# Optimization experiments

Measured on AMD Instinct MI355X. Metric: run time of the kernel, lower is better.

Reference implementation:

```python
import jax, jax.numpy as jnp
import numpy as np

D_MODEL = 512
D_STATE = 16
D_CONV = 4
EXPAND = 2
HEADDIM = 64
D_INNER = EXPAND * D_MODEL            # 1024
NHEADS = D_INNER // HEADDIM           # 16
CONV_DIM = D_INNER + 2 * D_STATE      # 1056 (x, B, C channels)
D_IN_PROJ = 2 * D_INNER + 2 * D_STATE + NHEADS  # 2096
EPS = 1e-5
B_SZ, L_SEQ = 8, 4096


def _mamba_param_keys(prefix):
    return [prefix + n for n in
            ('in_proj', 'conv_w', 'conv_b', 'dt_bias', 'A_log', 'D', 'norm_w', 'out_proj')]


def _make_mamba_params(key, prefix):
    ks = jax.random.split(key, 4)
    s = 0.02
    return {
        prefix + 'in_proj': jax.random.normal(ks[0], (D_IN_PROJ, D_MODEL), jnp.float32) * s,
        prefix + 'conv_w': jax.random.normal(ks[1], (CONV_DIM, D_CONV), jnp.float32) * s,
        prefix + 'conv_b': jnp.zeros((CONV_DIM,), jnp.float32),
        prefix + 'dt_bias': jax.random.normal(ks[2], (NHEADS,), jnp.float32) * 0.1,
        prefix + 'A_log': jnp.log(jnp.arange(1, NHEADS + 1, dtype=jnp.float32)),
        prefix + 'D': jnp.ones((NHEADS,), jnp.float32),
        prefix + 'norm_w': jnp.ones((D_INNER,), jnp.float32),
        prefix + 'out_proj': jax.random.normal(ks[3], (D_MODEL, D_INNER), jnp.float32) * s,
    }


def setup_inputs() -> dict:
    key = jax.random.key(0)
    kx, kf, kb, kp = jax.random.split(key, 4)
    inp = {'x': jax.random.normal(kx, (B_SZ, L_SEQ, D_MODEL), jnp.float32)}
    inp.update(_make_mamba_params(kf, 'f_'))
    inp.update(_make_mamba_params(kb, 'b_'))
    kp1, kp2 = jax.random.split(kp)
    inp['proj_w'] = jax.random.normal(kp1, (D_MODEL, 2 * D_MODEL), jnp.float32) * 0.02
    inp['proj_b'] = jnp.zeros((D_MODEL,), jnp.float32)
    inp['ln_w'] = jnp.ones((D_MODEL,), jnp.float32)
    inp['ln_b'] = jnp.zeros((D_MODEL,), jnp.float32)
    return inp


def mamba2(x, in_proj, conv_w, conv_b, dt_bias, A_log, Dp, norm_w, out_proj):
    """Mamba2 block (ngroups=1): in_proj -> causal depthwise conv -> selective scan -> gated RMSNorm -> out_proj."""
    B, L, _ = x.shape
    zxbcdt = x @ in_proj.T                               # [B,L,2096]
    z = zxbcdt[..., :D_INNER]                            # gate
    xBC = zxbcdt[..., D_INNER:D_INNER + CONV_DIM]
    dt = jax.nn.softplus(zxbcdt[..., D_INNER + CONV_DIM:] + dt_bias)  # [B,L,H]
    # causal depthwise conv over (x, B, C) channels + SiLU
    xp = jnp.pad(xBC, ((0, 0), (D_CONV - 1, 0), (0, 0)))
    conv = conv_b + sum(xp[:, k:k + L, :] * conv_w[:, k] for k in range(D_CONV))
    xBC = jax.nn.silu(conv)
    xs = xBC[..., :D_INNER].reshape(B, L, NHEADS, HEADDIM)  # [B,L,H,P]
    Bm = xBC[..., D_INNER:D_INNER + D_STATE]                # [B,L,N]
    Cm = xBC[..., D_INNER + D_STATE:]                       # [B,L,N]
    A = -jnp.exp(A_log)                                     # [H]
    dA = jnp.exp(dt * A)                                    # [B,L,H]

    def step(h, inp):
        dA_t, dt_t, x_t, B_t, C_t = inp                     # [B,H],[B,H],[B,H,P],[B,N],[B,N]
        h = h * dA_t[..., None, None] + (dt_t[..., None] * x_t)[..., None] * B_t[:, None, None, :]
        y = jnp.einsum('bhpn,bn->bhp', h, C_t)
        return h, y

    h0 = jnp.zeros((B, NHEADS, HEADDIM, D_STATE), x.dtype)
    inps = (dA.transpose(1, 0, 2), dt.transpose(1, 0, 2), xs.transpose(1, 0, 2, 3),
            Bm.transpose(1, 0, 2), Cm.transpose(1, 0, 2))
    _, ys = jax.lax.scan(step, h0, inps)                    # ys: [L,B,H,P]
    y = ys.transpose(1, 0, 2, 3) + Dp[:, None] * xs         # skip connection
    y = y.reshape(B, L, D_INNER)
    # gated RMSNorm (norm_before_gate=False)
    y = y * jax.nn.silu(z)
    y = y * jax.lax.rsqrt(jnp.mean(y * y, axis=-1, keepdims=True) + EPS) * norm_w
    return y @ out_proj.T


def _layer_norm(x, w, b):
    mu = jnp.mean(x, axis=-1, keepdims=True)
    v = jnp.var(x, axis=-1, keepdims=True)
    return (x - mu) * jax.lax.rsqrt(v + EPS) * w + b


def reference(x,
              f_in_proj, f_conv_w, f_conv_b, f_dt_bias, f_A_log, f_D, f_norm_w, f_out_proj,
              b_in_proj, b_conv_w, b_conv_b, b_dt_bias, b_A_log, b_D, b_norm_w, b_out_proj,
              proj_w, proj_b, ln_w, ln_b):
    x_fwd = mamba2(x, f_in_proj, f_conv_w, f_conv_b, f_dt_bias, f_A_log, f_D, f_norm_w, f_out_proj)
    x_bwd = jnp.flip(
        mamba2(jnp.flip(x, axis=1), b_in_proj, b_conv_w, b_conv_b, b_dt_bias, b_A_log, b_D, b_norm_w, b_out_proj),
        axis=1)
    comb = jnp.concatenate([x_fwd, x_bwd], axis=-1)         # [B,L,2D]
    out = comb @ proj_w.T + proj_b                          # dropout is identity (eval / p=0)
    return _layer_norm(x + out, ln_w, ln_b)
```

## Files before the change

kernel.cpp:

```cpp
#include <hip/hip_runtime.h>
#include <hip/hip_bf16.h>
#include <math.h>

typedef __bf16 bf16x8_t __attribute__((ext_vector_type(8)));
typedef float f32x4_t __attribute__((ext_vector_type(4)));
typedef unsigned short u16x8_t __attribute__((ext_vector_type(8)));
typedef unsigned short u16x4_t __attribute__((ext_vector_type(4)));

#define DEV __device__ __forceinline__

DEV float bf2f(unsigned short u) {
    unsigned int v = ((unsigned int)u) << 16;
    return __builtin_bit_cast(float, v);
}
DEV unsigned short f2bf(float f) {
    unsigned int u = __builtin_bit_cast(unsigned int, f);
    u += 0x7fffu + ((u >> 16) & 1u);
    return (unsigned short)(u >> 16);
}

__global__ __launch_bounds__(256) void cvt_k(
    const float* __restrict__ in, unsigned short* __restrict__ out, int n8)
{
    int t = blockIdx.x * 256 + threadIdx.x;
    if (t >= n8) return;
    f32x4_t a = ((const f32x4_t*)in)[t * 2];
    f32x4_t b = ((const f32x4_t*)in)[t * 2 + 1];
    u16x8_t o;
#pragma unroll
    for (int j = 0; j < 4; j++) { o[j] = f2bf(a[j]); o[4 + j] = f2bf(b[j]); }
    ((u16x8_t*)out)[t] = o;
}

template <bool FLIP_A, bool FLIP_C, bool OUT_F32, bool ADD_BIAS, bool ACCUM>
__global__ __launch_bounds__(256, 2) void gemm_bt(
    const unsigned short* __restrict__ A,
    const unsigned short* __restrict__ W,
    void* __restrict__ Cout,
    const float* __restrict__ bias,
    int N, int K, int ldc, int col_ofs)
{
    __shared__ __attribute__((aligned(16))) unsigned char smem[16384];
    const int tid  = threadIdx.x;
    const int wave = tid >> 6;
    const int lane = tid & 63;
    const int mtile = blockIdx.y << 7;
    const int ntile = blockIdx.x << 7;

    const int c0 = tid, c1 = 256 + tid;
    const int r0 = c0 >> 2, p0 = c0 & 3, g0 = p0 ^ ((r0 >> 1) & 3);
    const int r1 = c1 >> 2, p1 = c1 & 3, g1 = p1 ^ ((r1 >> 1) & 3);

    int am0 = mtile + r0; if (FLIP_A) am0 ^= 4095;
    int am1 = mtile + r1; if (FLIP_A) am1 ^= 4095;
    const unsigned short* aP0 = A + (size_t)am0 * K + g0 * 8;
    const unsigned short* aP1 = A + (size_t)am1 * K + g1 * 8;

    int wr0 = ntile + r0; if (wr0 > N - 1) wr0 = N - 1;
    int wr1 = ntile + r1; if (wr1 > N - 1) wr1 = N - 1;
    const unsigned short* wP0 = W + (size_t)wr0 * K + g0 * 8;
    const unsigned short* wP1 = W + (size_t)wr1 * K + g1 * 8;

    unsigned char* ldsA = smem;
    unsigned char* ldsW = smem + 8192;
    unsigned char* ldsA0 = ldsA + wave * 1024;
    unsigned char* ldsA1 = ldsA + 4096 + wave * 1024;
    unsigned char* ldsW0 = ldsW + wave * 1024;
    unsigned char* ldsW1 = ldsW + 4096 + wave * 1024;

    f32x4_t acc[4][4] = {};

    const int wm = (wave & 1) << 6;
    const int wn = (wave >> 1) << 6;
    const int r    = lane & 15;
    const int quad = lane >> 4;
    const int sw   = (r >> 1) & 3;

    int aoff[4], woff[4];
#pragma unroll
    for (int i = 0; i < 4; i++) {
        int m = wm + i * 16 + r;
        aoff[i] = (m * 4 + (quad ^ sw)) * 16;
        int n = wn + i * 16 + r;
        woff[i] = (n * 4 + (quad ^ sw)) * 16;
    }

    for (int k0 = 0; k0 < K; k0 += 32) {
        __builtin_amdgcn_global_load_lds(
            (const __attribute__((address_space(1))) void*)(aP0 + k0),
            (__attribute__((address_space(3))) void*)ldsA0, 16, 0, 0);
        __builtin_amdgcn_global_load_lds(
            (const __attribute__((address_space(1))) void*)(aP1 + k0),
            (__attribute__((address_space(3))) void*)ldsA1, 16, 0, 0);
        __builtin_amdgcn_global_load_lds(
            (const __attribute__((address_space(1))) void*)(wP0 + k0),
            (__attribute__((address_space(3))) void*)ldsW0, 16, 0, 0);
        __builtin_amdgcn_global_load_lds(
            (const __attribute__((address_space(1))) void*)(wP1 + k0),
            (__attribute__((address_space(3))) void*)ldsW1, 16, 0, 0);
        __syncthreads();

        bf16x8_t af[4], wf[4];
#pragma unroll
        for (int i = 0; i < 4; i++)
            af[i] = __builtin_bit_cast(bf16x8_t, *(const u16x8_t*)(ldsA + aoff[i]));
#pragma unroll
        for (int j = 0; j < 4; j++)
            wf[j] = __builtin_bit_cast(bf16x8_t, *(const u16x8_t*)(ldsW + woff[j]));
#pragma unroll
        for (int i = 0; i < 4; i++)
#pragma unroll
            for (int j = 0; j < 4; j++)
                acc[i][j] = __builtin_amdgcn_mfma_f32_16x16x32_bf16(af[i], wf[j], acc[i][j], 0, 0, 0);
        __syncthreads();
    }

#pragma unroll
    for (int i = 0; i < 4; i++) {
#pragma unroll
        for (int j = 0; j < 4; j++) {
            int cc = ntile + wn + j * 16 + r;
            if (cc >= N) continue;
#pragma unroll
            for (int reg = 0; reg < 4; reg++) {
                int rr = mtile + wm + i * 16 + quad * 4 + reg;
                int orow = FLIP_C ? (rr ^ 4095) : rr;
                float v = acc[i][j][reg];
                if (ADD_BIAS) v += bias[cc];
                if (OUT_F32) {
                    float* p = (float*)Cout + (size_t)orow * ldc + col_ofs + cc;
                    if (ACCUM) v += *p;
                    *p = v;
                } else {
                    ((unsigned short*)Cout)[(size_t)orow * ldc + col_ofs + cc] = f2bf(v);
                }
            }
        }
    }
}

__global__ __launch_bounds__(256) void eprep2_k(
    const float* __restrict__ pw,
    const float* __restrict__ op0,
    const float* __restrict__ op1,
    unsigned short* __restrict__ E)
{
    const int dir = blockIdx.y;
    const int n0  = blockIdx.x << 2;
    const int k4  = threadIdx.x;
    const float* op  = dir ? op1 : op0;
    const float* pwr = pw + (size_t)n0 * 1024 + (dir ? 512 : 0);
    const float* opc = op + (k4 << 2);

    float acc[4][4] = {};
#pragma unroll 8
    for (int j = 0; j < 512; j++) {
        f32x4_t o = *(const f32x4_t*)(opc + ((size_t)j << 10));
        float w0 = pwr[j];
        float w1 = pwr[1024 + j];
        float w2 = pwr[2048 + j];
        float w3 = pwr[3072 + j];
#pragma unroll
        for (int q = 0; q < 4; q++) {
            acc[0][q] = fmaf(w0, o[q], acc[0][q]);
            acc[1][q] = fmaf(w1, o[q], acc[1][q]);
            acc[2][q] = fmaf(w2, o[q], acc[2][q]);
            acc[3][q] = fmaf(w3, o[q], acc[3][q]);
        }
    }

    unsigned short* Ed = E + (size_t)dir * 512 * 1024;
#pragma unroll
    for (int i = 0; i < 4; i++) {
        u16x4_t e;
#pragma unroll
        for (int q = 0; q < 4; q++) e[q] = f2bf(acc[i][q]);
        *(u16x4_t*)(Ed + (size_t)(n0 + i) * 1024 + (k4 << 2)) = e;
    }
}

__global__ __launch_bounds__(256) void conv_silu_k(
    const unsigned short* __restrict__ xin,
    const float* __restrict__ cw,
    const float* __restrict__ cb,
    unsigned short* __restrict__ outp)
{
    int t = blockIdx.x * 256 + threadIdx.x;
    int c8 = t % 132;
    int rb = t / 132;
    int c = c8 * 8;
    int row0 = rb * 8;
    int l0 = row0 & 4095;

    float w[8][4];
#pragma unroll
    for (int j = 0; j < 8; j++) {
        f32x4_t wv = *(const f32x4_t*)(cw + (c + j) * 4);
        w[j][0] = wv[0]; w[j][1] = wv[1]; w[j][2] = wv[2]; w[j][3] = wv[3];
    }
    float bia[8];
    {
        f32x4_t b0 = *(const f32x4_t*)(cb + c);
        f32x4_t b1 = *(const f32x4_t*)(cb + c + 4);
#pragma unroll
        for (int j = 0; j < 4; j++) { bia[j] = b0[j]; bia[4 + j] = b1[j]; }
    }

    u16x8_t zero;
#pragma unroll
    for (int j = 0; j < 8; j++) zero[j] = 0;

    u16x8_t win[11];
#pragma unroll
    for (int u = 0; u < 11; u++) {
        int lu = l0 - 3 + u;
        win[u] = (lu >= 0)
            ? *(const u16x8_t*)(xin + (size_t)(row0 - 3 + u) * 1072 + c)
            : zero;
    }

#pragma unroll
    for (int s = 0; s < 8; s++) {
        float acc[8];
#pragma unroll
        for (int j = 0; j < 8; j++) acc[j] = bia[j];
#pragma unroll
        for (int k = 0; k < 4; k++) {
            u16x8_t xv = win[s + k];
#pragma unroll
            for (int j = 0; j < 8; j++)
                acc[j] = fmaf(bf2f(xv[j]), w[j][k], acc[j]);
        }
        u16x8_t o;
#pragma unroll
        for (int j = 0; j < 8; j++) {
            float xx = acc[j];
            o[j] = f2bf(xx * __builtin_amdgcn_rcpf(1.f + __expf(-xx)));
        }
        *(u16x8_t*)(outp + (size_t)(row0 + s) * 1056 + c) = o;
    }
}

__global__ __launch_bounds__(256) void dt_pre_k(
    const unsigned short* __restrict__ xin,
    const float* __restrict__ dt_bias,
    const float* __restrict__ A_log,
    float* __restrict__ dtb, float* __restrict__ ldab)
{
    int t = blockIdx.x * 256 + threadIdx.x;
    int h = t & 15;
    int row = t >> 4;
    float x = bf2f(xin[(size_t)row * 1072 + 1056 + h]) + dt_bias[h];
    float dt = (x > 20.f) ? x : log1pf(__expf(x));
    float A = -__expf(A_log[h]);
    dtb[t] = dt;
    ldab[t] = dt * A;
}

DEV void stage_xt(const unsigned short* __restrict__ xrow, unsigned short* XtW, int l)
{
    u16x8_t xv[8];
#pragma unroll
    for (int m = 0; m < 8; m++) xv[m] = *(const u16x8_t*)(xrow + m * 8);
#pragma unroll
    for (int p = 0; p < 64; p++) {
        int blkc = (l >> 3) ^ (p & 7);
        XtW[p * 64 + blkc * 8 + (l & 7)] = xv[p >> 3][p & 7];
    }
}

DEV bf16x8_t xt_frag(const unsigned short* XtW, int r, int quad, int jj, int kk)
{
    int p = jj * 16 + r;
    int blkc = (kk * 4 + quad) ^ (p & 7);
    return __builtin_bit_cast(bf16x8_t, *(const u16x8_t*)(XtW + p * 64 + blkc * 8));
}

__global__ __launch_bounds__(256) void scan_chstate_k(
    const unsigned short* __restrict__ xc,
    const float* __restrict__ dtb,
    float* __restrict__ lcs,
    float* __restrict__ Hend, float* __restrict__ dec)
{
    __shared__ __attribute__((aligned(16))) unsigned char sm[37120];
    unsigned short* Btr = (unsigned short*)sm;
    float* csW = (float*)(sm + 2304);
    float* dtW = (float*)(sm + 3328);
    unsigned short* Xt0 = (unsigned short*)(sm + 4352);

    const int tid = threadIdx.x;
    const int w = tid >> 6, l = tid & 63;
    const int r = l & 15, quad = l >> 4;
    const int row0 = blockIdx.x * 64;
    const int b = blockIdx.x >> 6, chunk = blockIdx.x & 63;
    const int h = blockIdx.y * 4 + w;
    const int blk = ((b * 16 + h) << 6) | chunk;

    {
        int n = tid & 15, s0 = (tid >> 4) * 4;
#pragma unroll
        for (int js = 0; js < 4; js++) {
            int s = s0 + js;
            Btr[n * 72 + s] = xc[(size_t)(row0 + s) * 1056 + 1024 + n];
        }
    }

    float v   = lcs[(size_t)(row0 + l) * 16 + h];
    float dtv = dtb[(size_t)(row0 + l) * 16 + h];
#pragma unroll
    for (int d = 1; d < 64; d <<= 1) {
        float o = __shfl_up(v, d, 64);
        if (l >= d) v += o;
    }
    lcs[(size_t)(row0 + l) * 16 + h] = v;
    csW[w * 64 + l] = v;
    dtW[w * 64 + l] = dtv;
    if (l == 63) dec[blk] = __expf(v);
    __syncthreads();

    unsigned short* XtW = Xt0 + w * 4096;
    stage_xt(xc + (size_t)(row0 + l) * 1056 + h * 64, XtW, l);

    const float* csr = csW + w * 64;
    const float* dtr = dtW + w * 64;
    float cs63 = csr[63];

    f32x4_t z = {0.f, 0.f, 0.f, 0.f};
    f32x4_t hacc[4] = {z, z, z, z};
#pragma unroll
    for (int kk = 0; kk < 2; kk++) {
        int sb = kk * 32 + quad * 8;
        u16x8_t bv = *(const u16x8_t*)(Btr + r * 72 + sb);
        f32x4_t c0 = *(const f32x4_t*)(csr + sb);
        f32x4_t c1 = *(const f32x4_t*)(csr + sb + 4);
        f32x4_t d0 = *(const f32x4_t*)(dtr + sb);
        f32x4_t d1 = *(const f32x4_t*)(dtr + sb + 4);
        u16x8_t wv;
#pragma unroll
        for (int j = 0; j < 4; j++) {
            wv[j]     = f2bf(bf2f(bv[j])     * d0[j] * __expf(cs63 - c0[j]));
            wv[4 + j] = f2bf(bf2f(bv[4 + j]) * d1[j] * __expf(cs63 - c1[j]));
        }
        bf16x8_t wf = __builtin_bit_cast(bf16x8_t, wv);
#pragma unroll
        for (int jj = 0; jj < 4; jj++)
            hacc[jj] = __builtin_amdgcn_mfma_f32_16x16x32_bf16(wf, xt_frag(XtW, r, quad, jj, kk), hacc[jj], 0, 0, 0);
    }
    float* o = Hend + (size_t)blk * 1024;
#pragma unroll
    for (int jj = 0; jj < 4; jj++)
#pragma unroll
        for (int reg = 0; reg < 4; reg++)
            o[(jj * 16 + r) * 16 + quad * 4 + reg] = hacc[jj][reg];
}

__global__ __launch_bounds__(64) void scan_comb_k(float* __restrict__ H, const float* __restrict__ dec)
{
    int bh = blockIdx.x >> 2;
    int q  = blockIdx.x & 3;
    int t  = threadIdx.x;
    float* base = H + (size_t)bh * 64 * 1024 + q * 256 + t * 4;
    const float* dp = dec + bh * 64;
    f32x4_t hs = {0.f, 0.f, 0.f, 0.f};
    f32x4_t cur = *(const f32x4_t*)base;
    for (int c = 0; c < 64; c++) {
        int cn = (c < 63) ? c + 1 : 63;
        f32x4_t nxt = *(const f32x4_t*)(base + (size_t)cn * 1024);
        float d = dp[c];
        *(f32x4_t*)(base + (size_t)c * 1024) = hs;
#pragma unroll
        for (int j = 0; j < 4; j++) hs[j] = fmaf(hs[j], d, cur[j]);
        cur = nxt;
    }
}

__global__ __launch_bounds__(256) void scan_chout_k(
    const unsigned short* __restrict__ xc,
    const float* __restrict__ dtb, const float* __restrict__ csb,
    const float* __restrict__ Hst, const float* __restrict__ Dp,
    unsigned short* __restrict__ ybuf)
{
    __shared__ __attribute__((aligned(16))) unsigned char sm[60416];
    unsigned short* Ct = (unsigned short*)sm;
    unsigned short* Bt = (unsigned short*)(sm + 4096);
    float* S   = (float*)(sm + 8192);
    float* csL = (float*)(sm + 25600);
    float* dtL = (float*)(sm + 26624);
    unsigned short* Xt0 = (unsigned short*)(sm + 27648);

    const int tid = threadIdx.x;
    const int w = tid >> 6, l = tid & 63;
    const int r = l & 15, quad = l >> 4;
    const int row0 = blockIdx.x * 64;
    const int b = blockIdx.x >> 6, chunk = blockIdx.x & 63;
    const int h = blockIdx.y * 4 + w;
    const int blk = ((b * 16 + h) << 6) | chunk;

    {
        int rowi = tid >> 2, seg = tid & 3;
        u16x8_t vb, vc;
        if (seg < 2) {
            const unsigned short* src = xc + (size_t)(row0 + rowi) * 1056 + 1024 + seg * 8;
            vb = *(const u16x8_t*)src;
            vc = *(const u16x8_t*)(src + 16);
        } else {
#pragma unroll
            for (int j = 0; j < 8; j++) { vb[j] = 0; vc[j] = 0; }
        }
        *(u16x8_t*)(Bt + rowi * 32 + seg * 8) = vb;
        *(u16x8_t*)(Ct + rowi * 32 + seg * 8) = vc;
    }
    csL[w * 64 + l] = csb[(size_t)(row0 + l) * 16 + h];
    dtL[w * 64 + l] = dtb[(size_t)(row0 + l) * 16 + h];
    __syncthreads();

    {
        bf16x8_t cf = __builtin_bit_cast(bf16x8_t, *(const u16x8_t*)(Ct + (w * 16 + r) * 32 + quad * 8));
        f32x4_t z = {0.f, 0.f, 0.f, 0.f};
#pragma unroll
        for (int j = 0; j < 4; j++) {
            bf16x8_t bfv = __builtin_bit_cast(bf16x8_t, *(const u16x8_t*)(Bt + (j * 16 + r) * 32 + quad * 8));
            f32x4_t d = __builtin_amdgcn_mfma_f32_16x16x32_bf16(cf, bfv, z, 0, 0, 0);
#pragma unroll
            for (int reg = 0; reg < 4; reg++)
                S[(w * 16 + quad * 4 + reg) * 68 + j * 16 + r] = d[reg];
        }
    }
    __syncthreads();

    unsigned short* XtW = Xt0 + w * 4096;
    stage_xt(xc + (size_t)(row0 + l) * 1056 + h * 64, XtW, l);

    const float* csr = csL + w * 64;
    const float* dtr = dtL + w * 64;

    f32x4_t acc[4][4];
    {
        bf16x8_t hf[4];
#pragma unroll
        for (int jj = 0; jj < 4; jj++) {
            int p = jj * 16 + r;
            u16x8_t hv;
            if (quad < 2) {
                const float* hp = Hst + (size_t)blk * 1024 + p * 16 + quad * 8;
                f32x4_t h0 = *(const f32x4_t*)hp;
                f32x4_t h1 = *(const f32x4_t*)(hp + 4);
#pragma unroll
                for (int j = 0; j < 4; j++) { hv[j] = f2bf(h0[j]); hv[4 + j] = f2bf(h1[j]); }
            } else {
#pragma unroll
                for (int j = 0; j < 8; j++) hv[j] = 0;
            }
            hf[jj] = __builtin_bit_cast(bf16x8_t, hv);
        }
        f32x4_t z = {0.f, 0.f, 0.f, 0.f};
#pragma unroll
        for (int i = 0; i < 4; i++) {
            bf16x8_t cf = __builtin_bit_cast(bf16x8_t, *(const u16x8_t*)(Ct + (i * 16 + r) * 32 + quad * 8));
#pragma unroll
            for (int jj = 0; jj < 4; jj++)
                acc[i][jj] = __builtin_amdgcn_mfma_f32_16x16x32_bf16(cf, hf[jj], z, 0, 0, 0);
        }
#pragma unroll
        for (int i = 0; i < 4; i++) {
            f32x4_t es;
#pragma unroll
            for (int reg = 0; reg < 4; reg++) es[reg] = __expf(csr[i * 16 + quad * 4 + reg]);
#pragma unroll
            for (int jj = 0; jj < 4; jj++)
#pragma unroll
                for (int reg = 0; reg < 4; reg++) acc[i][jj][reg] *= es[reg];
        }
    }

#pragma unroll
    for (int kk = 0; kk < 2; kk++) {
        int sb = kk * 32 + quad * 8;
        bf16x8_t xf[4];
#pragma unroll
        for (int jj = 0; jj < 4; jj++) xf[jj] = xt_frag(XtW, r, quad, jj, kk);
        f32x4_t c0 = *(const f32x4_t*)(csr + sb);
        f32x4_t c1 = *(const f32x4_t*)(csr + sb + 4);
        f32x4_t d0 = *(const f32x4_t*)(dtr + sb);
        f32x4_t d1 = *(const f32x4_t*)(dtr + sb + 4);
#pragma unroll
        for (int i = 0; i < 4; i++) {
            int t = i * 16 + r;
            float cst = csr[t];
            const float* Srow = S + t * 68;
            f32x4_t s0 = *(const f32x4_t*)(Srow + sb);
            f32x4_t s1 = *(const f32x4_t*)(Srow + sb + 4);
            u16x8_t wv;
#pragma unroll
            for (int j = 0; j < 4; j++) {
                int s = sb + j;
                float v0 = (s <= t) ? __expf(cst - c0[j]) * d0[j] * s0[j] : 0.f;
                wv[j] = f2bf(v0);
                int s2 = sb + 4 + j;
                float v1 = (s2 <= t) ? __expf(cst - c1[j]) * d1[j] * s1[j] : 0.f;
                wv[4 + j] = f2bf(v1);
            }
            bf16x8_t wf = __builtin_bit_cast(bf16x8_t, wv);
#pragma unroll
            for (int jj = 0; jj < 4; jj++)
                acc[i][jj] = __builtin_amdgcn_mfma_f32_16x16x32_bf16(wf, xf[jj], acc[i][jj], 0, 0, 0);
        }
    }

    float Dh = Dp[h];
#pragma unroll
    for (int i = 0; i < 4; i++) {
#pragma unroll
        for (int jj = 0; jj < 4; jj++) {
            int p = jj * 16 + r;
            int t0 = i * 16 + quad * 4;
            int blk2 = (t0 >> 3) ^ (p & 7);
            u16x4_t x4 = *(const u16x4_t*)(XtW + p * 64 + blk2 * 8 + (t0 & 7));
#pragma unroll
            for (int reg = 0; reg < 4; reg++) {
                float yv = fmaf(Dh, bf2f(x4[reg]), acc[i][jj][reg]);
                ybuf[(size_t)(row0 + t0 + reg) * 1024 + h * 64 + p] = f2bf(yv);
            }
        }
    }
}

__global__ __launch_bounds__(256) void rmsgate_k(
    unsigned short* __restrict__ y,
    const unsigned short* __restrict__ z,
    const float* __restrict__ nw)
{
    __shared__ float sred[256];
    int row = blockIdx.x;
    int t = threadIdx.x;
    int c = t * 4;
    u16x4_t yv = *(const u16x4_t*)(y + (size_t)row * 1024 + c);
    u16x4_t zv = *(const u16x4_t*)(z + (size_t)row * 1024 + c);
    float g[4];
    float ss = 0.f;
#pragma unroll
    for (int j = 0; j < 4; j++) {
        float zf = bf2f(zv[j]);
        float sil = zf * __builtin_amdgcn_rcpf(1.f + __expf(-zf));
        g[j] = bf2f(yv[j]) * sil;
        ss += g[j] * g[j];
    }
    sred[t] = ss;
    __syncthreads();
#pragma unroll
    for (int s = 128; s > 0; s >>= 1) {
        if (t < s) sred[t] += sred[t + s];
        __syncthreads();
    }
    float scale = rsqrtf(sred[0] * (1.f / 1024.f) + 1e-5f);
    u16x4_t o4;
#pragma unroll
    for (int j = 0; j < 4; j++) o4[j] = f2bf(g[j] * scale * nw[c + j]);
    *(u16x4_t*)(y + (size_t)row * 1024 + c) = o4;
}

__global__ __launch_bounds__(128) void ln_k(
    const float* __restrict__ x,
    const float* __restrict__ f,
    const float* __restrict__ lw,
    const float* __restrict__ lb,
    float* __restrict__ outp)
{
    __shared__ float sA[128], sB[128];
    int row = blockIdx.x;
    int t = threadIdx.x;
    int c = t * 4;
    float s[4];
    float sum = 0.f, sq = 0.f;
    f32x4_t xv = *(const f32x4_t*)(x + (size_t)row * 512 + c);
    f32x4_t fv = *(const f32x4_t*)(f + (size_t)row * 512 + c);
#pragma unroll
    for (int j = 0; j < 4; j++) {
        s[j] = xv[j] + fv[j];
        sum += s[j];
        sq += s[j] * s[j];
    }
    sA[t] = sum; sB[t] = sq;
    __syncthreads();
#pragma unroll
    for (int st = 64; st > 0; st >>= 1) {
        if (t < st) { sA[t] += sA[t + st]; sB[t] += sB[t + st]; }
        __syncthreads();
    }
    float mu = sA[0] * (1.f / 512.f);
    float var = sB[0] * (1.f / 512.f) - mu * mu;
    if (var < 0.f) var = 0.f;
    float inv = rsqrtf(var + 1e-5f);
    f32x4_t o4;
#pragma unroll
    for (int j = 0; j < 4; j++)
        o4[j] = (s[j] - mu) * inv * lw[c + j] + lb[c + j];
    *(f32x4_t*)(outp + (size_t)row * 512 + c) = o4;
}

extern "C" void kernel_launch(void* const* d_in, const int* in_sizes, int n_in,
                              void* d_out, int out_size, void* d_ws, size_t ws_size,
                              hipStream_t stream)
{
    (void)in_sizes; (void)n_in; (void)out_size;

    const float* x           = (const float*)d_in[0];
    const float* in_proj[2]  = {(const float*)d_in[1],  (const float*)d_in[9]};
    const float* conv_w[2]   = {(const float*)d_in[2],  (const float*)d_in[10]};
    const float* conv_b[2]   = {(const float*)d_in[3],  (const float*)d_in[11]};
    const float* dt_bias[2]  = {(const float*)d_in[4],  (const float*)d_in[12]};
    const float* A_log[2]    = {(const float*)d_in[5],  (const float*)d_in[13]};
    const float* Dp[2]       = {(const float*)d_in[6],  (const float*)d_in[14]};
    const float* norm_w[2]   = {(const float*)d_in[7],  (const float*)d_in[15]};
    const float* out_proj[2] = {(const float*)d_in[8],  (const float*)d_in[16]};
    const float* proj_w      = (const float*)d_in[17];
    const float* proj_b      = (const float*)d_in[18];
    const float* ln_w        = (const float*)d_in[19];
    const float* ln_b        = (const float*)d_in[20];
    float* outp = (float*)d_out;

    const size_t IP_ELEMS = (size_t)2096 * 512;
    const size_t X_ELEMS  = (size_t)32768 * 512;

    const size_t constBytes = X_ELEMS * 2 + 2 * IP_ELEMS * 2 + 2 * 512 * 1024 * 2 + 4096;
    int g = 1;
    {
        const int cands[3] = {8, 4, 2};
        for (int ci = 0; ci < 3; ci++) {
            size_t R = (size_t)cands[ci] * 4096;
            size_t need = constBytes + R * (2144 + 2112 + 2048 + 64 + 64 + 1024)
                        + (size_t)cands[ci] * 1024 * 4 + 16 * 256;
            if (need <= ws_size) { g = cands[ci]; break; }
        }
    }
    const size_t R = (size_t)g * 4096;
    const int nGroups = 8 / g;
    const int MT = (int)(R >> 7);

    char* ws = (char*)d_ws;
    size_t off = 0;
    auto alloc = [&](size_t bytes) -> char* {
        char* p = ws + off;
        off += (bytes + 255) & ~(size_t)255;
        return p;
    };
    unsigned short* xb16  = (unsigned short*)alloc(X_ELEMS * 2);
    unsigned short* ipb16[2];
    ipb16[0] = (unsigned short*)alloc(IP_ELEMS * 2);
    ipb16[1] = (unsigned short*)alloc(IP_ELEMS * 2);
    unsigned short* Ebuf  = (unsigned short*)alloc(2 * 512 * 1024 * 2);
    unsigned short* Ef    = Ebuf;
    unsigned short* Eb    = Ebuf + 512 * 1024;
    unsigned short* xbcdt = (unsigned short*)alloc(R * 1072 * 2);
    unsigned short* ybuf  = xbcdt;
    unsigned short* xconv = (unsigned short*)alloc(R * 1056 * 2);
    unsigned short* zbuf  = xconv;
    float* fbuf = (float*)alloc(R * 512 * 4);
    float* dtb  = (float*)alloc(R * 16 * 4);
    float* dab  = (float*)alloc(R * 16 * 4);
    float* Hbuf = (float*)alloc(R * 1024);
    float* dec  = (float*)alloc((size_t)g * 1024 * 4);

    dim3 blk(256);

    cvt_k<<<(unsigned)((X_ELEMS / 8 + 255) / 256), blk, 0, stream>>>(x, xb16, (int)(X_ELEMS / 8));
    cvt_k<<<(unsigned)((IP_ELEMS / 8 + 255) / 256), blk, 0, stream>>>(in_proj[0], ipb16[0], (int)(IP_ELEMS / 8));
    cvt_k<<<(unsigned)((IP_ELEMS / 8 + 255) / 256), blk, 0, stream>>>(in_proj[1], ipb16[1], (int)(IP_ELEMS / 8));
    eprep2_k<<<dim3(128, 2), blk, 0, stream>>>(proj_w, out_proj[0], out_proj[1], Ebuf);

    for (int grp = 0; grp < nGroups; grp++) {
        const unsigned short* xg = xb16 + (size_t)grp * R * 512;
        const float* xgf = x + (size_t)grp * R * 512;
        float* og = outp + (size_t)grp * R * 512;

        for (int dir = 0; dir < 2; dir++) {
            if (dir == 0)
                gemm_bt<false, false, false, false, false><<<dim3(9, MT), blk, 0, stream>>>(
                    xg, ipb16[0] + (size_t)1024 * 512, xbcdt, nullptr, 1072, 512, 1072, 0);
            else
                gemm_bt<true, false, false, false, false><<<dim3(9, MT), blk, 0, stream>>>(
                    xg, ipb16[1] + (size_t)1024 * 512, xbcdt, nullptr, 1072, 512, 1072, 0);

            conv_silu_k<<<(unsigned)(R * 132 / 2048), blk, 0, stream>>>(xbcdt, conv_w[dir], conv_b[dir], xconv);
            dt_pre_k<<<(unsigned)(R * 16 / 256), blk, 0, stream>>>(xbcdt, dt_bias[dir], A_log[dir], dtb, dab);

            scan_chstate_k<<<dim3((unsigned)(R / 64), 4), blk, 0, stream>>>(xconv, dtb, dab, Hbuf, dec);
            scan_comb_k<<<(unsigned)(g * 64), dim3(64), 0, stream>>>(Hbuf, dec);
            scan_chout_k<<<dim3((unsigned)(R / 64), 4), blk, 0, stream>>>(xconv, dtb, dab, Hbuf, Dp[dir], ybuf);

            if (dir == 0)
                gemm_bt<false, false, false, false, false><<<dim3(8, MT), blk, 0, stream>>>(
                    xg, ipb16[0], zbuf, nullptr, 1024, 512, 1024, 0);
            else
                gemm_bt<true, false, false, false, false><<<dim3(8, MT), blk, 0, stream>>>(
                    xg, ipb16[1], zbuf, nullptr, 1024, 512, 1024, 0);

            rmsgate_k<<<(unsigned)R, blk, 0, stream>>>(ybuf, zbuf, norm_w[dir]);

            if (dir == 0)
                gemm_bt<false, false, true, true, false><<<dim3(4, MT), blk, 0, stream>>>(
                    ybuf, Ef, fbuf, proj_b, 512, 1024, 512, 0);
            else
                gemm_bt<false, true, true, false, true><<<dim3(4, MT), blk, 0, stream>>>(
                    ybuf, Eb, fbuf, nullptr, 512, 1024, 512, 0);
        }
        ln_k<<<(unsigned)R, dim3(128), 0, stream>>>(xgf, fbuf, ln_w, ln_b, og);
    }
}
```

Baseline: 964.1 us.

## Compute fused projection weights with MFMA GEMM and use wave-per-row norms

Replaces the scalar eprep2 kernel, which folded proj_w into out_proj, with a bf16 packing of proj_w, a tiled transpose of out_proj and two small gemm_bt launches on the matrix cores. The RMS-gate and LayerNorm kernels now give each row to one 64-lane wave and reduce with cross-lane shuffles instead of a shared-memory tree with repeated barriers. Loads and stores are widened to 8 or 16 elements per lane. The weight precompute gains bf16 rounding of its inputs before the matmul, and the added workspace buffers can change which group size fits.

```diff
diff --git a/kernel.cpp b/kernel.cpp
--- a/kernel.cpp
+++ b/kernel.cpp
@@ -139,43 +139,43 @@
     }
 }
 
-__global__ __launch_bounds__(256) void eprep2_k(
-    const float* __restrict__ pw,
-    const float* __restrict__ op0,
-    const float* __restrict__ op1,
-    unsigned short* __restrict__ E)
-{
-    const int dir = blockIdx.y;
-    const int n0  = blockIdx.x << 2;
-    const int k4  = threadIdx.x;
-    const float* op  = dir ? op1 : op0;
-    const float* pwr = pw + (size_t)n0 * 1024 + (dir ? 512 : 0);
-    const float* opc = op + (k4 << 2);
-
-    float acc[4][4] = {};
-#pragma unroll 8
-    for (int j = 0; j < 512; j++) {
-        f32x4_t o = *(const f32x4_t*)(opc + ((size_t)j << 10));
-        float w0 = pwr[j];
-        float w1 = pwr[1024 + j];
-        float w2 = pwr[2048 + j];
-        float w3 = pwr[3072 + j];
-#pragma unroll
-        for (int q = 0; q < 4; q++) {
-            acc[0][q] = fmaf(w0, o[q], acc[0][q]);
-            acc[1][q] = fmaf(w1, o[q], acc[1][q]);
-            acc[2][q] = fmaf(w2, o[q], acc[2][q]);
-            acc[3][q] = fmaf(w3, o[q], acc[3][q]);
-        }
-    }
-
-    unsigned short* Ed = E + (size_t)dir * 512 * 1024;
+__global__ __launch_bounds__(256) void pack_pw_k(
+    const float* __restrict__ pw, unsigned short* __restrict__ pwb)
+{
+    int t = blockIdx.x * 256 + threadIdx.x;
+    int j8 = t & 63;
+    int n  = (t >> 6) & 511;
+    int dir = t >> 15;
+    const float* src = pw + (size_t)n * 1024 + dir * 512 + j8 * 8;
+    f32x4_t a = *(const f32x4_t*)src;
+    f32x4_t b = *(const f32x4_t*)(src + 4);
+    u16x8_t o;
+#pragma unroll
+    for (int j = 0; j < 4; j++) { o[j] = f2bf(a[j]); o[4 + j] = f2bf(b[j]); }
+    *(u16x8_t*)(pwb + (size_t)dir * 512 * 512 + (size_t)n * 512 + j8 * 8) = o;
+}
+
+__global__ __launch_bounds__(256) void tr_op_k(
+    const float* __restrict__ op0, const float* __restrict__ op1,
+    unsigned short* __restrict__ opT)
+{
+    __shared__ float tile[32][33];
+    const int dir = blockIdx.z;
+    const float* op = dir ? op1 : op0;
+    const int k0 = blockIdx.x * 32;
+    const int j0 = blockIdx.y * 32;
+    const int tx = threadIdx.x & 31, ty = threadIdx.x >> 5;
 #pragma unroll
     for (int i = 0; i < 4; i++) {
-        u16x4_t e;
-#pragma unroll
-        for (int q = 0; q < 4; q++) e[q] = f2bf(acc[i][q]);
-        *(u16x4_t*)(Ed + (size_t)(n0 + i) * 1024 + (k4 << 2)) = e;
+        int j = j0 + ty + i * 8;
+        tile[ty + i * 8][tx] = op[(size_t)j * 1024 + k0 + tx];
+    }
+    __syncthreads();
+    unsigned short* dst = opT + (size_t)dir * 1024 * 512;
+#pragma unroll
+    for (int i = 0; i < 4; i++) {
+        int k = k0 + ty + i * 8;
+        dst[(size_t)k * 512 + j0 + tx] = f2bf(tile[tx][ty + i * 8]);
     }
 }
 
@@ -530,72 +530,94 @@
     const unsigned short* __restrict__ z,
     const float* __restrict__ nw)
 {
-    __shared__ float sred[256];
-    int row = blockIdx.x;
-    int t = threadIdx.x;
-    int c = t * 4;
-    u16x4_t yv = *(const u16x4_t*)(y + (size_t)row * 1024 + c);
-    u16x4_t zv = *(const u16x4_t*)(z + (size_t)row * 1024 + c);
-    float g[4];
+    const int wave = threadIdx.x >> 6, lane = threadIdx.x & 63;
+    const size_t row = (size_t)blockIdx.x * 4 + wave;
+    const int c = lane * 16;
+    unsigned short* yp = y + row * 1024 + c;
+    const unsigned short* zp = z + row * 1024 + c;
+    u16x8_t yv0 = *(const u16x8_t*)yp;
+    u16x8_t yv1 = *(const u16x8_t*)(yp + 8);
+    u16x8_t zv0 = *(const u16x8_t*)zp;
+    u16x8_t zv1 = *(const u16x8_t*)(zp + 8);
+    float g[16];
     float ss = 0.f;
 #pragma unroll
+    for (int j = 0; j < 8; j++) {
+        float zf = bf2f(zv0[j]);
+        float sil = zf * __builtin_amdgcn_rcpf(1.f + __expf(-zf));
+        g[j] = bf2f(yv0[j]) * sil;
+        ss += g[j] * g[j];
+    }
+#pragma unroll
+    for (int j = 0; j < 8; j++) {
+        float zf = bf2f(zv1[j]);
+        float sil = zf * __builtin_amdgcn_rcpf(1.f + __expf(-zf));
+        g[8 + j] = bf2f(yv1[j]) * sil;
+        ss += g[8 + j] * g[8 + j];
+    }
+#pragma unroll
+    for (int m = 32; m > 0; m >>= 1) ss += __shfl_xor(ss, m, 64);
+    float scale = rsqrtf(ss * (1.f / 1024.f) + 1e-5f);
+    f32x4_t w0 = *(const f32x4_t*)(nw + c);
+    f32x4_t w1 = *(const f32x4_t*)(nw + c + 4);
+    f32x4_t w2 = *(const f32x4_t*)(nw + c + 8);
+    f32x4_t w3 = *(const f32x4_t*)(nw + c + 12);
+    u16x8_t o0, o1;
+#pragma unroll
     for (int j = 0; j < 4; j++) {
-        float zf = bf2f(zv[j]);
-        float sil = zf * __builtin_amdgcn_rcpf(1.f + __expf(-zf));
-        g[j] = bf2f(yv[j]) * sil;
-        ss += g[j] * g[j];
-    }
-    sred[t] = ss;
-    __syncthreads();
-#pragma unroll
-    for (int s = 128; s > 0; s >>= 1) {
-        if (t < s) sred[t] += sred[t + s];
-        __syncthreads();
-    }
-    float scale = rsqrtf(sred[0] * (1.f / 1024.f) + 1e-5f);
-    u16x4_t o4;
-#pragma unroll
-    for (int j = 0; j < 4; j++) o4[j] = f2bf(g[j] * scale * nw[c + j]);
-    *(u16x4_t*)(y + (size_t)row * 1024 + c) = o4;
-}
-
-__global__ __launch_bounds__(128) void ln_k(
+        o0[j]     = f2bf(g[j]      * scale * w0[j]);
+        o0[4 + j] = f2bf(g[4 + j]  * scale * w1[j]);
+        o1[j]     = f2bf(g[8 + j]  * scale * w2[j]);
+        o1[4 + j] = f2bf(g[12 + j] * scale * w3[j]);
+    }
+    *(u16x8_t*)yp = o0;
+    *(u16x8_t*)(yp + 8) = o1;
+}
+
+__global__ __launch_bounds__(256) void ln_k(
     const float* __restrict__ x,
     const float* __restrict__ f,
     const float* __restrict__ lw,
     const float* __restrict__ lb,
     float* __restrict__ outp)
 {
-    __shared__ float sA[128], sB[128];
-    int row = blockIdx.x;
-    int t = threadIdx.x;
-    int c = t * 4;
-    float s[4];
+    const int wave = threadIdx.x >> 6, lane = threadIdx.x & 63;
+    const size_t row = (size_t)blockIdx.x * 4 + wave;
+    const int c = lane * 8;
+    f32x4_t xv0 = *(const f32x4_t*)(x + row * 512 + c);
+    f32x4_t xv1 = *(const f32x4_t*)(x + row * 512 + c + 4);
+    f32x4_t fv0 = *(const f32x4_t*)(f + row * 512 + c);
+    f32x4_t fv1 = *(const f32x4_t*)(f + row * 512 + c + 4);
+    float s[8];
     float sum = 0.f, sq = 0.f;
-    f32x4_t xv = *(const f32x4_t*)(x + (size_t)row * 512 + c);
-    f32x4_t fv = *(const f32x4_t*)(f + (size_t)row * 512 + c);
 #pragma unroll
     for (int j = 0; j < 4; j++) {
-        s[j] = xv[j] + fv[j];
-        sum += s[j];
-        sq += s[j] * s[j];
-    }
-    sA[t] = sum; sB[t] = sq;
-    __syncthreads();
-#pragma unroll
-    for (int st = 64; st > 0; st >>= 1) {
-        if (t < st) { sA[t] += sA[t + st]; sB[t] += sB[t + st]; }
-        __syncthreads();
-    }
-    float mu = sA[0] * (1.f / 512.f);
-    float var = sB[0] * (1.f / 512.f) - mu * mu;
+        s[j] = xv0[j] + fv0[j];
+        s[4 + j] = xv1[j] + fv1[j];
+    }
+#pragma unroll
+    for (int j = 0; j < 8; j++) { sum += s[j]; sq += s[j] * s[j]; }
+#pragma unroll
+    for (int m = 32; m > 0; m >>= 1) {
+        sum += __shfl_xor(sum, m, 64);
+        sq  += __shfl_xor(sq, m, 64);
+    }
+    float mu = sum * (1.f / 512.f);
+    float var = sq * (1.f / 512.f) - mu * mu;
     if (var < 0.f) var = 0.f;
     float inv = rsqrtf(var + 1e-5f);
-    f32x4_t o4;
-#pragma unroll
-    for (int j = 0; j < 4; j++)
-        o4[j] = (s[j] - mu) * inv * lw[c + j] + lb[c + j];
-    *(f32x4_t*)(outp + (size_t)row * 512 + c) = o4;
+    f32x4_t w0 = *(const f32x4_t*)(lw + c);
+    f32x4_t w1 = *(const f32x4_t*)(lw + c + 4);
+    f32x4_t b0 = *(const f32x4_t*)(lb + c);
+    f32x4_t b1 = *(const f32x4_t*)(lb + c + 4);
+    f32x4_t o0, o1;
+#pragma unroll
+    for (int j = 0; j < 4; j++) {
+        o0[j] = (s[j] - mu) * inv * w0[j] + b0[j];
+        o1[j] = (s[4 + j] - mu) * inv * w1[j] + b1[j];
+    }
+    *(f32x4_t*)(outp + row * 512 + c) = o0;
+    *(f32x4_t*)(outp + row * 512 + c + 4) = o1;
 }
 
 extern "C" void kernel_launch(void* const* d_in, const int* in_sizes, int n_in,
@@ -622,7 +644,8 @@
     const size_t IP_ELEMS = (size_t)2096 * 512;
     const size_t X_ELEMS  = (size_t)32768 * 512;
 
-    const size_t constBytes = X_ELEMS * 2 + 2 * IP_ELEMS * 2 + 2 * 512 * 1024 * 2 + 4096;
+    const size_t constBytes = X_ELEMS * 2 + 2 * IP_ELEMS * 2 + 2 * 512 * 1024 * 2
+                            + 2 * 512 * 512 * 2 + 2 * 1024 * 512 * 2 + 8192;
     int g = 1;
     {
         const int cands[3] = {8, 4, 2};
@@ -651,6 +674,8 @@
     unsigned short* Ebuf  = (unsigned short*)alloc(2 * 512 * 1024 * 2);
     unsigned short* Ef    = Ebuf;
     unsigned short* Eb    = Ebuf + 512 * 1024;
+    unsigned short* pwb   = (unsigned short*)alloc(2 * 512 * 512 * 2);
+    unsigned short* opT   = (unsigned short*)alloc(2 * 1024 * 512 * 2);
     unsigned short* xbcdt = (unsigned short*)alloc(R * 1072 * 2);
     unsigned short* ybuf  = xbcdt;
     unsigned short* xconv = (unsigned short*)alloc(R * 1056 * 2);
@@ -666,7 +691,12 @@
     cvt_k<<<(unsigned)((X_ELEMS / 8 + 255) / 256), blk, 0, stream>>>(x, xb16, (int)(X_ELEMS / 8));
     cvt_k<<<(unsigned)((IP_ELEMS / 8 + 255) / 256), blk, 0, stream>>>(in_proj[0], ipb16[0], (int)(IP_ELEMS / 8));
     cvt_k<<<(unsigned)((IP_ELEMS / 8 + 255) / 256), blk, 0, stream>>>(in_proj[1], ipb16[1], (int)(IP_ELEMS / 8));
-    eprep2_k<<<dim3(128, 2), blk, 0, stream>>>(proj_w, out_proj[0], out_proj[1], Ebuf);
+    pack_pw_k<<<256, blk, 0, stream>>>(proj_w, pwb);
+    tr_op_k<<<dim3(32, 16, 2), blk, 0, stream>>>(out_proj[0], out_proj[1], opT);
+    gemm_bt<false, false, false, false, false><<<dim3(8, 4), blk, 0, stream>>>(
+        pwb, opT, Ef, nullptr, 1024, 512, 1024, 0);
+    gemm_bt<false, false, false, false, false><<<dim3(8, 4), blk, 0, stream>>>(
+        pwb + 512 * 512, opT + 1024 * 512, Eb, nullptr, 1024, 512, 1024, 0);
 
     for (int grp = 0; grp < nGroups; grp++) {
         const unsigned short* xg = xb16 + (size_t)grp * R * 512;
@@ -695,7 +725,7 @@
                 gemm_bt<true, false, false, false, false><<<dim3(8, MT), blk, 0, stream>>>(
                     xg, ipb16[1], zbuf, nullptr, 1024, 512, 1024, 0);
 
-            rmsgate_k<<<(unsigned)R, blk, 0, stream>>>(ybuf, zbuf, norm_w[dir]);
+            rmsgate_k<<<(unsigned)(R / 4), blk, 0, stream>>>(ybuf, zbuf, norm_w[dir]);
 
             if (dir == 0)
                 gemm_bt<false, false, true, true, false><<<dim3(4, MT), blk, 0, stream>>>(
@@ -704,6 +734,6 @@
                 gemm_bt<false, true, true, false, true><<<dim3(4, MT), blk, 0, stream>>>(
                     ybuf, Eb, fbuf, nullptr, 512, 1024, 512, 0);
         }
-        ln_k<<<(unsigned)R, dim3(128), 0, stream>>>(xgf, fbuf, ln_w, ln_b, og);
-    }
-}
+        ln_k<<<(unsigned)(R / 4), blk, 0, stream>>>(xgf, fbuf, ln_w, ln_b, og);
+    }
+}
```

Result: no change. 952.3 us (-1.2%).
